# Optimization experiments

Hardware: AMD Instinct MI355X
Metric: run time of the kernel (lower is better)

Reference implementation:

```python
import jax, jax.numpy as jnp
import numpy as np

N_NODES = 50000

def cheb_conv(x, edge_index, W, b):
    # PyG ChebConv, K=2, normalization='sym', lambda_max=2.0 (default):
    # scaled Laplacian L_hat = (2/lambda_max)*L - I = -D^{-1/2} A D^{-1/2} (zero diag).
    # Tx_0 = x, Tx_1 = L_hat @ x ; out = Tx_0 @ W[0] + Tx_1 @ W[1] + b
    src, dst = edge_index[0], edge_index[1]
    ones = jnp.ones(src.shape[0], x.dtype)
    deg = jax.ops.segment_sum(ones, src, num_segments=N_NODES)
    dinv = jnp.where(deg > 0, 1.0 / jnp.sqrt(deg), 0.0)
    norm = -dinv[src] * dinv[dst]                                   # [E]
    tx1 = jax.ops.segment_sum(x[src] * norm[:, None], dst, num_segments=N_NODES)
    return x @ W[0] + tx1 @ W[1] + b

def setup_inputs() -> dict:
    key = jax.random.key(0)
    ks = jax.random.split(key, 12)
    IN, OUT, E, P = 128, 2, 800000, 400000
    return {
        "x": jax.random.normal(ks[0], (N_NODES, IN), jnp.float32),
        "edge_index": jax.random.randint(ks[1], (2, E), 0, N_NODES),
        "E_pos": jax.random.randint(ks[2], (2, P), 0, N_NODES),
        "neg_edge_index": jax.random.randint(ks[3], (2, P), 0, N_NODES),
        "W1": jax.random.normal(ks[4], (2, IN, 300), jnp.float32) * 0.05,
        "b1": jnp.zeros((300,), jnp.float32),
        "W2": jax.random.normal(ks[5], (2, 300, 100), jnp.float32) * 0.05,
        "b2": jnp.zeros((100,), jnp.float32),
        "W3": jax.random.normal(ks[6], (2, 100, OUT), jnp.float32) * 0.05,
        "b3": jnp.zeros((OUT,), jnp.float32),
        "lin1_W": jax.random.normal(ks[7], (100, IN), jnp.float32) * 0.05,
        "lin1_b": jnp.zeros((100,), jnp.float32),
        "lin2_W": jax.random.normal(ks[8], (100, IN), jnp.float32) * 0.05,
        "lin2_b": jnp.zeros((100,), jnp.float32),
        "c1": jnp.full((1,), 0.5, jnp.float32),
        "c2": jnp.full((1,), 0.5, jnp.float32),
    }

def reference(x, edge_index, E_pos, neg_edge_index, W1, b1, W2, b2, W3, b3,
              lin1_W, lin1_b, lin2_W, lin2_b, c1, c2):
    # eval mode: F.dropout and dropout_edge are identity
    x0 = x
    h = jax.nn.relu(cheb_conv(x0, edge_index, W1, b1))
    x1 = jax.nn.relu(cheb_conv(h, edge_index, W2, b2))
    x2 = x1 + jax.nn.relu(x0 @ lin1_W.T + lin1_b)
    z = x1 + jax.nn.relu(x0 @ lin2_W.T + lin2_b)
    pos_score = jnp.sum(z[E_pos[0]] * z[E_pos[1]], axis=1)              # [P]
    pos_loss = -jnp.mean(jnp.log(jax.nn.sigmoid(pos_score) + 1e-15))
    neg_score = jnp.sum(z[neg_edge_index[0]] * z[neg_edge_index[1]], axis=1)
    neg_loss = -jnp.mean(jnp.log(1.0 - jax.nn.sigmoid(neg_score) + 1e-15))
    r_loss = pos_loss + neg_loss
    out = cheb_conv(x2, edge_index, W3, b3)                             # [N, out_channels]
    return (out, r_loss, c1, c2)
```

## Files before the change

### kernel.cpp

```cpp
#include <hip/hip_runtime.h>
#include <math.h>


typedef unsigned short ushort_t;
typedef unsigned char u8;
typedef __attribute__((ext_vector_type(8))) __bf16 bf16x8;
typedef __attribute__((ext_vector_type(8))) short s16x8;
typedef __attribute__((ext_vector_type(4))) float f32x4;
typedef __attribute__((ext_vector_type(2))) float f32x2;

#define NB_H 64
#define HW 12500

__device__ __forceinline__ f32x4 mfma16x16x32(s16x8 a, s16x8 b, f32x4 c) {
  return __builtin_amdgcn_mfma_f32_16x16x32_bf16(
      __builtin_bit_cast(bf16x8, a), __builtin_bit_cast(bf16x8, b), c, 0, 0, 0);
}
__device__ __forceinline__ ushort_t f2bf(float f) {
  union { float f; unsigned u; } c; c.f = f;
  unsigned r = (c.u + 0x7FFFu + ((c.u >> 16) & 1u)) >> 16;
  return (ushort_t)r;
}
__device__ __forceinline__ f32x2 cvt2lo(unsigned u) {
  return __builtin_amdgcn_cvt_pk_f32_fp8((int)u, false);
}
__device__ __forceinline__ f32x2 cvt2hi(unsigned u) {
  return __builtin_amdgcn_cvt_pk_f32_fp8((int)u, true);
}
__device__ __forceinline__ u8 f2fp8(float f) {
  return (u8)(__builtin_amdgcn_cvt_pk_fp8_f32(f, 0.f, 0, false) & 0xff);
}

template<int VAR, int NT, int KTOT>
__global__ __launch_bounds__(256) void gemm_mfma(
    const ushort_t* __restrict__ A0, const ushort_t* __restrict__ A1,
    const ushort_t* __restrict__ Wt,
    const float* __restrict__ bias0, const float* __restrict__ bias1,
    const float* __restrict__ x1,
    const float* __restrict__ W3c, const float* __restrict__ b3c,
    void* __restrict__ out0, void* __restrict__ out1,
    float* __restrict__ t0g, float* __restrict__ t1g, int M,
    int gemmNB,
    const int* __restrict__ ep, const int* __restrict__ en, int P,
    const int* __restrict__ pptr, const unsigned* __restrict__ baseP,
    const ushort_t* __restrict__ prank, int2* __restrict__ psr)
{
  if (VAR == 0 && (int)blockIdx.x >= gemmNB) {
    const int i = ((int)blockIdx.x - gemmNB) * 256 + (int)threadIdx.x;
    const int twoP = 2 * P;
    if (i >= twoP) return;
    const int neg = (i >= P);
    const int p = neg ? i - P : i;
    const int* ia = neg ? en : ep;
    const int na = ia[p], nbv = ia[P + p];
    const int cs2 = (twoP + NB_H - 1) / NB_H;
    const int b = i / cs2;
    const unsigned bv = baseP[(size_t)b * HW + (na >> 2)];
    const int base = (int)((bv >> ((na & 3) * 8)) & 0xffu);
    const int pos = pptr[na] + base + (int)prank[i];
    psr[pos] = make_int2(na, nbv | (neg ? (int)0x80000000 : 0));
    return;
  }
  constexpr int NF = NT / 32;
  __shared__ __align__(16) ushort_t As[64 * 40];
  __shared__ __align__(16) ushort_t Bs[NT * 40];
  __shared__ float w3s[400];
  const int tid  = threadIdx.x;
  const int lane = tid & 63, w = tid >> 6;
  const int m0 = blockIdx.x * 64;
  const int wm = (w & 1) * 32, wn = (w >> 1) * (NT / 2);
  if (VAR == 2) { for (int i = tid; i < 400; i += 256) w3s[i] = W3c[i]; }
  f32x4 acc[2][NF];
#pragma unroll
  for (int i = 0; i < 2; ++i)
#pragma unroll
    for (int j = 0; j < NF; ++j) acc[i][j] = (f32x4){0.f, 0.f, 0.f, 0.f};

  for (int k0 = 0; k0 < KTOT; k0 += 32) {
    {
      const int r = tid >> 2, c8 = (tid & 3) * 8;
      const int gm = m0 + r;
      uint4 v = {0u, 0u, 0u, 0u};
      if (gm < M) {
        if (VAR == 1) {
          const u8* s8 = (const u8*)A0 + (size_t)gm * 320 + k0 + c8;
          const uint2 r8 = *(const uint2*)s8;
          const f32x2 f0 = cvt2lo(r8.x), f1 = cvt2hi(r8.x);
          const f32x2 f2 = cvt2lo(r8.y), f3 = cvt2hi(r8.y);
          v.x = (unsigned)f2bf(f0.x) | ((unsigned)f2bf(f0.y) << 16);
          v.y = (unsigned)f2bf(f1.x) | ((unsigned)f2bf(f1.y) << 16);
          v.z = (unsigned)f2bf(f2.x) | ((unsigned)f2bf(f2.y) << 16);
          v.w = (unsigned)f2bf(f3.x) | ((unsigned)f2bf(f3.y) << 16);
        } else {
          const ushort_t* srcp;
          if (VAR == 0) srcp = (k0 < 128) ? A0 + (size_t)gm * 128 + k0 + c8
                                          : A1 + (size_t)gm * 128 + (k0 - 128) + c8;
          else srcp = A0 + (size_t)gm * 128 + k0 + c8;
          v = *(const uint4*)srcp;
        }
      }
      *(uint4*)&As[r * 40 + c8] = v;
    }
    {
      const int c8 = (tid & 3) * 8;
#pragma unroll
      for (int i = 0; i < (NT * 4 + 255) / 256; ++i) {
        const int r = (tid >> 2) + i * 64;
        if (r < NT)
          *(uint4*)&Bs[r * 40 + c8] = *(const uint4*)(Wt + (size_t)r * KTOT + k0 + c8);
      }
    }
    __syncthreads();
    s16x8 af[2], bfr[NF];
#pragma unroll
    for (int mi = 0; mi < 2; ++mi)
      af[mi] = *(const s16x8*)&As[(wm + mi * 16 + (lane & 15)) * 40 + (lane >> 4) * 8];
#pragma unroll
    for (int ni = 0; ni < NF; ++ni)
      bfr[ni] = *(const s16x8*)&Bs[(wn + ni * 16 + (lane & 15)) * 40 + (lane >> 4) * 8];
#pragma unroll
    for (int mi = 0; mi < 2; ++mi)
#pragma unroll
      for (int ni = 0; ni < NF; ++ni)
        acc[mi][ni] = mfma16x16x32(af[mi], bfr[ni], acc[mi][ni]);
    __syncthreads();
  }

  if (VAR == 2) {
#pragma unroll
    for (int mi = 0; mi < 2; ++mi)
#pragma unroll
      for (int r = 0; r < 4; ++r) {
        const int gRow = m0 + wm + mi * 16 + ((lane >> 4) << 2) + r;
        float p0 = 0.f, p1 = 0.f, p2 = 0.f, p3 = 0.f;
#pragma unroll
        for (int ni = 0; ni < NF; ++ni) {
          const int col = wn + ni * 16 + (lane & 15);
          const float v = acc[mi][ni][r];
          if (gRow < M) {
            if (col < 100) {
              const float x2v = x1[(size_t)gRow * 128 + col] + fmaxf(v + bias0[col], 0.f);
              p0 = fmaf(x2v, w3s[col * 2 + 0], p0);
              p1 = fmaf(x2v, w3s[col * 2 + 1], p1);
              p2 = fmaf(x2v, w3s[200 + col * 2 + 0], p2);
              p3 = fmaf(x2v, w3s[200 + col * 2 + 1], p3);
            } else if (col < 200) {
              const int c = col - 100;
              ((u8*)out1)[(size_t)gRow * 128 + c] =
                  f2fp8(x1[(size_t)gRow * 128 + c] + fmaxf(v + bias1[c], 0.f));
            }
          }
        }
        if (wn == 0) {
#pragma unroll
          for (int off = 8; off; off >>= 1) {
            p0 += __shfl_down(p0, off, 16);
            p1 += __shfl_down(p1, off, 16);
            p2 += __shfl_down(p2, off, 16);
            p3 += __shfl_down(p3, off, 16);
          }
          if ((lane & 15) == 0 && gRow < M) {
            t0g[(size_t)gRow * 2 + 0] = p0 + b3c[0];
            t0g[(size_t)gRow * 2 + 1] = p1 + b3c[1];
            t1g[(size_t)gRow * 2 + 0] = p2;
            t1g[(size_t)gRow * 2 + 1] = p3;
          }
        }
      }
  } else {
#pragma unroll
    for (int mi = 0; mi < 2; ++mi)
#pragma unroll
      for (int ni = 0; ni < NF; ++ni)
#pragma unroll
        for (int r = 0; r < 4; ++r) {
          const int gRow = m0 + wm + mi * 16 + ((lane >> 4) << 2) + r;
          const int col  = wn + ni * 16 + (lane & 15);
          if (gRow >= M) continue;
          const float v = acc[mi][ni][r];
          if (VAR == 0) {
            ((u8*)out0)[(size_t)gRow * 320 + col] =
                (col < 300) ? f2fp8(fmaxf(v + bias0[col], 0.f)) : (u8)0;
          } else {
            if (col < 100) ((float*)out0)[(size_t)gRow * 128 + col] = v + bias0[col];
            else if (col < 200) ((u8*)out1)[(size_t)gRow * 128 + (col - 100)] = f2fp8(v);
          }
        }
  }
}

__global__ __launch_bounds__(256) void prep(
    const int* __restrict__ src, const int* __restrict__ dst, int E, int M,
    unsigned* __restrict__ partS, unsigned* __restrict__ partD,
    ushort_t* __restrict__ rank,
    const int* __restrict__ ep, const int* __restrict__ en, int P,
    unsigned* __restrict__ partP, ushort_t* __restrict__ prank,
    const float* __restrict__ x, ushort_t* __restrict__ xb,
    u8* __restrict__ xf8, int n4,
    const float* __restrict__ W1, const float* __restrict__ W2,
    const float* __restrict__ l1W, const float* __restrict__ l2W,
    ushort_t* __restrict__ W1t, ushort_t* __restrict__ W2t,
    ushort_t* __restrict__ Wlt)
{
  __shared__ unsigned hist[HW];
  const int blk = blockIdx.x;
  if (blk < 2 * NB_H) {
    const int isD = (blk >= NB_H);
    const int b = isD ? blk - NB_H : blk;
    const int* keys = isD ? dst : src;
    unsigned* part = isD ? partD : partS;
    const int cs = (E + NB_H - 1) / NB_H;
    const int e0 = b * cs;
    const int e1 = (e0 + cs < E) ? e0 + cs : E;
    for (int i = threadIdx.x; i < HW; i += 256) hist[i] = 0;
    __syncthreads();
    for (int e = e0 + threadIdx.x; e < e1; e += 256) {
      const int k = keys[e];
      const unsigned old = atomicAdd(&hist[k >> 2], 1u << ((k & 3) * 8));
      if (isD) rank[e] = (ushort_t)((old >> ((k & 3) * 8)) & 0xffu);
    }
    __syncthreads();
    for (int i = threadIdx.x; i < HW; i += 256)
      part[(size_t)b * HW + i] = hist[i];
    return;
  }
  if (blk < 3 * NB_H) {
    const int b = blk - 2 * NB_H;
    const int twoP = 2 * P;
    const int cs2 = (twoP + NB_H - 1) / NB_H;
    const int e0 = b * cs2;
    const int e1 = (e0 + cs2 < twoP) ? e0 + cs2 : twoP;
    for (int i = threadIdx.x; i < HW; i += 256) hist[i] = 0;
    __syncthreads();
    for (int i = e0 + threadIdx.x; i < e1; i += 256) {
      const int neg = (i >= P);
      const int p = neg ? i - P : i;
      const int* ia = neg ? en : ep;
      const int k = ia[p];
      const unsigned old = atomicAdd(&hist[k >> 2], 1u << ((k & 3) * 8));
      prank[i] = (ushort_t)((old >> ((k & 3) * 8)) & 0xffu);
    }
    __syncthreads();
    for (int i = threadIdx.x; i < HW; i += 256)
      partP[(size_t)b * HW + i] = hist[i];
    return;
  }
  const int i = (blk - 3 * NB_H) * 256 + threadIdx.x;
  if (i < n4) {
    const float4 v = ((const float4*)x)[i];
    ushort4 o; o.x = f2bf(v.x); o.y = f2bf(v.y); o.z = f2bf(v.z); o.w = f2bf(v.w);
    ((ushort4*)xb)[i] = o;
    int p = 0;
    p = __builtin_amdgcn_cvt_pk_fp8_f32(v.x, v.y, p, false);
    p = __builtin_amdgcn_cvt_pk_fp8_f32(v.z, v.w, p, true);
    ((unsigned*)xf8)[i] = (unsigned)p;
    return;
  }
  const int j = i - n4;
  if (j < 81920) {
    const int n = j >> 8, k = j & 255;
    float v = 0.f;
    if (n < 300) v = (k < 128) ? W1[k * 300 + n] : W1[38400 + (k - 128) * 300 + n];
    W1t[j] = f2bf(v);
  } else if (j < 153600) {
    const int jj = j - 81920;
    const int n = jj / 320, k = jj - n * 320;
    float v = 0.f;
    if (n < 200 && k < 300) v = W2[(n < 100 ? 0 : 30000) + k * 100 + (n % 100)];
    W2t[jj] = f2bf(v);
  } else if (j < 182272) {
    const int jj = j - 153600;
    const int n = jj >> 7, k = jj & 127;
    float v = 0.f;
    if (n < 100) v = l1W[n * 128 + k];
    else if (n < 200) v = l2W[(n - 100) * 128 + k];
    Wlt[jj] = f2bf(v);
  }
}

__global__ void scan_local(const unsigned* __restrict__ partS,
                           unsigned* __restrict__ partD,
                           unsigned* __restrict__ partP,
                           float* __restrict__ dinv,
                           int* __restrict__ ptr, int* __restrict__ pptr,
                           int* __restrict__ bsumE, int* __restrict__ bsumP, int n)
{
  __shared__ int tmp[256];
  const int i = blockIdx.x * 256 + threadIdx.x;
  const int lane = threadIdx.x & 63;
  unsigned ssum = 0, dtot = 0, ptot = 0;
  if (i < n && (i & 3) == 0) {
    const int c = i >> 2;
    for (int b = 0; b < NB_H; b += 8) {
      unsigned sv[8];
#pragma unroll
      for (int q = 0; q < 8; ++q) sv[q] = partS[(size_t)(b + q) * HW + c];
#pragma unroll
      for (int q = 0; q < 8; ++q) ssum += sv[q];
    }
    unsigned run = 0;
    for (int b = 0; b < NB_H; b += 8) {
      unsigned dv[8];
#pragma unroll
      for (int q = 0; q < 8; ++q) dv[q] = partD[(size_t)(b + q) * HW + c];
#pragma unroll
      for (int q = 0; q < 8; ++q) { const unsigned pre = run; run += dv[q]; dv[q] = pre; }
#pragma unroll
      for (int q = 0; q < 8; ++q) partD[(size_t)(b + q) * HW + c] = dv[q];
    }
    dtot = run;
    unsigned prun = 0;
    for (int b = 0; b < NB_H; b += 8) {
      unsigned pv[8];
#pragma unroll
      for (int q = 0; q < 8; ++q) pv[q] = partP[(size_t)(b + q) * HW + c];
#pragma unroll
      for (int q = 0; q < 8; ++q) { const unsigned pre = prun; prun += pv[q]; pv[q] = pre; }
#pragma unroll
      for (int q = 0; q < 8; ++q) partP[(size_t)(b + q) * HW + c] = pv[q];
    }
    ptot = prun;
  }
  const unsigned sAll = __shfl(ssum, lane & ~3, 64);
  const unsigned dAll = __shfl(dtot, lane & ~3, 64);
  const unsigned pAll = __shfl(ptot, lane & ~3, 64);
  int v = 0, v2 = 0;
  if (i < n) {
    const int hs = (i & 3) * 8;
    const unsigned dg = (sAll >> hs) & 0xffu;
    dinv[i] = dg ? 1.f / sqrtf((float)dg) : 0.f;
    v = (int)((dAll >> hs) & 0xffu);
    v2 = (int)((pAll >> hs) & 0xffu);
  }
  tmp[threadIdx.x] = v;
  __syncthreads();
  for (int off = 1; off < 256; off <<= 1) {
    const int t = (threadIdx.x >= off) ? tmp[threadIdx.x - off] : 0;
    __syncthreads();
    tmp[threadIdx.x] += t;
    __syncthreads();
  }
  if (i < n) ptr[i] = tmp[threadIdx.x] - v;
  if (threadIdx.x == 255) bsumE[blockIdx.x] = tmp[255];
  __syncthreads();
  tmp[threadIdx.x] = v2;
  __syncthreads();
  for (int off = 1; off < 256; off <<= 1) {
    const int t = (threadIdx.x >= off) ? tmp[threadIdx.x - off] : 0;
    __syncthreads();
    tmp[threadIdx.x] += t;
    __syncthreads();
  }
  if (i < n) pptr[i] = tmp[threadIdx.x] - v2;
  if (threadIdx.x == 255) bsumP[blockIdx.x] = tmp[255];
}

__global__ void scan_add2(int* __restrict__ ptr, int* __restrict__ pptr,
                          const int* __restrict__ bsumE, const int* __restrict__ bsumP,
                          int n, int E, int twoP, int nb, float* __restrict__ accs)
{
  __shared__ int tmp[256];
  const int v = (threadIdx.x < nb) ? bsumE[threadIdx.x] : 0;
  tmp[threadIdx.x] = v;
  __syncthreads();
  for (int off = 1; off < 256; off <<= 1) {
    const int t = (threadIdx.x >= off) ? tmp[threadIdx.x - off] : 0;
    __syncthreads();
    tmp[threadIdx.x] += t;
    __syncthreads();
  }
  const int offE = (blockIdx.x > 0) ? tmp[blockIdx.x - 1] : 0;
  __syncthreads();
  const int v2 = (threadIdx.x < nb) ? bsumP[threadIdx.x] : 0;
  tmp[threadIdx.x] = v2;
  __syncthreads();
  for (int off = 1; off < 256; off <<= 1) {
    const int t = (threadIdx.x >= off) ? tmp[threadIdx.x - off] : 0;
    __syncthreads();
    tmp[threadIdx.x] += t;
    __syncthreads();
  }
  const int offP = (blockIdx.x > 0) ? tmp[blockIdx.x - 1] : 0;
  const int i = blockIdx.x * 256 + threadIdx.x;
  if (i < n) { ptr[i] += offE; pptr[i] += offP; }
  if (i == 0) { ptr[n] = E; pptr[n] = twoP; accs[0] = 0.f; accs[1] = 0.f; }
}

__global__ void fill_csr2(const int* __restrict__ src, const int* __restrict__ dst,
                          const float* __restrict__ dinv, const int* __restrict__ ptr,
                          const unsigned* __restrict__ baseD,
                          const ushort_t* __restrict__ rank,
                          int2* __restrict__ csr, int E)
{
  const int e = blockIdx.x * 256 + threadIdx.x;
  if (e >= E) return;
  const int cs = (E + NB_H - 1) / NB_H;
  const int b = e / cs;
  const int s = src[e], d = dst[e];
  const unsigned bv = baseD[(size_t)b * HW + (d >> 2)];
  const int base = (int)((bv >> ((d & 3) * 8)) & 0xffu);
  const int pos = ptr[d] + base + (int)rank[e];
  const float w = -dinv[s] * dinv[d];
  csr[pos] = make_int2(s, __float_as_int(w));
}

#define ACCV(u, ww) { f32x2 t; \
  t = cvt2lo(u.x); a[0]  = fmaf(ww, t.x, a[0]);  a[1]  = fmaf(ww, t.y, a[1]);  \
  t = cvt2hi(u.x); a[2]  = fmaf(ww, t.x, a[2]);  a[3]  = fmaf(ww, t.y, a[3]);  \
  t = cvt2lo(u.y); a[4]  = fmaf(ww, t.x, a[4]);  a[5]  = fmaf(ww, t.y, a[5]);  \
  t = cvt2hi(u.y); a[6]  = fmaf(ww, t.x, a[6]);  a[7]  = fmaf(ww, t.y, a[7]);  \
  t = cvt2lo(u.z); a[8]  = fmaf(ww, t.x, a[8]);  a[9]  = fmaf(ww, t.y, a[9]);  \
  t = cvt2hi(u.z); a[10] = fmaf(ww, t.x, a[10]); a[11] = fmaf(ww, t.y, a[11]); \
  t = cvt2lo(u.w); a[12] = fmaf(ww, t.x, a[12]); a[13] = fmaf(ww, t.y, a[13]); \
  t = cvt2hi(u.w); a[14] = fmaf(ww, t.x, a[14]); a[15] = fmaf(ww, t.y, a[15]); }

__global__ __launch_bounds__(256) void gather128e(
    const u8* __restrict__ xf8, ushort_t* __restrict__ txb,
    const int* __restrict__ ptr, const int2* __restrict__ csr, int M)
{
  const int node = (blockIdx.x * 256 + threadIdx.x) >> 3;
  const int sub  = threadIdx.x & 7;
  if (node >= M) return;
  const int beg = ptr[node], end = ptr[node + 1];
  float a[16] = {};
  int p = beg;
  for (; p + 8 <= end; p += 8) {
    int2 e[8];
#pragma unroll
    for (int q = 0; q < 8; ++q) e[q] = csr[p + q];
    uint4 v[8];
#pragma unroll
    for (int q = 0; q < 8; ++q)
      v[q] = *(const uint4*)(xf8 + (size_t)e[q].x * 128 + sub * 16);
#pragma unroll
    for (int q = 0; q < 8; ++q) { const float wq = __int_as_float(e[q].y); ACCV(v[q], wq) }
  }
  for (; p < end; ++p) {
    const int2 eq = csr[p]; const float wq = __int_as_float(eq.y);
    const uint4 v = *(const uint4*)(xf8 + (size_t)eq.x * 128 + sub * 16);
    ACCV(v, wq)
  }
  uint4 o1, o2;
  o1.x = (unsigned)f2bf(a[0])  | ((unsigned)f2bf(a[1])  << 16);
  o1.y = (unsigned)f2bf(a[2])  | ((unsigned)f2bf(a[3])  << 16);
  o1.z = (unsigned)f2bf(a[4])  | ((unsigned)f2bf(a[5])  << 16);
  o1.w = (unsigned)f2bf(a[6])  | ((unsigned)f2bf(a[7])  << 16);
  o2.x = (unsigned)f2bf(a[8])  | ((unsigned)f2bf(a[9])  << 16);
  o2.y = (unsigned)f2bf(a[10]) | ((unsigned)f2bf(a[11]) << 16);
  o2.z = (unsigned)f2bf(a[12]) | ((unsigned)f2bf(a[13]) << 16);
  o2.w = (unsigned)f2bf(a[14]) | ((unsigned)f2bf(a[15]) << 16);
  ushort_t* dstp = txb + (size_t)node * 128 + sub * 16;
  *(uint4*)dstp = o1;
  *(uint4*)(dstp + 8) = o2;
}

__global__ __launch_bounds__(256) void gather100e_x1(
    const u8* __restrict__ Brh, float* __restrict__ Ar,
    const int* __restrict__ ptr, const int2* __restrict__ csr, int M)
{
  const int node = (blockIdx.x * 256 + threadIdx.x) >> 3;
  const int sub  = threadIdx.x & 7;
  if (node >= M) return;
  const int beg = ptr[node], end = ptr[node + 1];
  float a[16] = {};
  int p = beg;
  for (; p + 8 <= end; p += 8) {
    int2 e[8];
#pragma unroll
    for (int q = 0; q < 8; ++q) e[q] = csr[p + q];
    uint4 v[8];
#pragma unroll
    for (int q = 0; q < 8; ++q)
      v[q] = *(const uint4*)(Brh + (size_t)e[q].x * 128 + sub * 16);
#pragma unroll
    for (int q = 0; q < 8; ++q) { const float wq = __int_as_float(e[q].y); ACCV(v[q], wq) }
  }
  for (; p < end; ++p) {
    const int2 eq = csr[p]; const float wq = __int_as_float(eq.y);
    const uint4 v = *(const uint4*)(Brh + (size_t)eq.x * 128 + sub * 16);
    ACCV(v, wq)
  }
  float* dstp = Ar + (size_t)node * 128 + sub * 16;
#pragma unroll
  for (int q = 0; q < 4; ++q) {
    float4 b = *(const float4*)(dstp + q * 4);
    b.x = fmaxf(b.x + a[q * 4 + 0], 0.f);
    b.y = fmaxf(b.y + a[q * 4 + 1], 0.f);
    b.z = fmaxf(b.z + a[q * 4 + 2], 0.f);
    b.w = fmaxf(b.w + a[q * 4 + 3], 0.f);
    *(float4*)(dstp + q * 4) = b;
  }
}
#undef ACCV

__device__ __forceinline__ void maskrow(uint4& r, int sub) {
  if (sub >= 6) { r.y = 0u; r.z = 0u; r.w = 0u; if (sub == 7) r.x = 0u; }
}
#define DOTA(vv, s) { f32x2 q_; \
  q_ = cvt2lo(vv.x); s = fmaf(af[0],  q_.x, s); s = fmaf(af[1],  q_.y, s); \
  q_ = cvt2hi(vv.x); s = fmaf(af[2],  q_.x, s); s = fmaf(af[3],  q_.y, s); \
  q_ = cvt2lo(vv.y); s = fmaf(af[4],  q_.x, s); s = fmaf(af[5],  q_.y, s); \
  q_ = cvt2hi(vv.y); s = fmaf(af[6],  q_.x, s); s = fmaf(af[7],  q_.y, s); \
  q_ = cvt2lo(vv.z); s = fmaf(af[8],  q_.x, s); s = fmaf(af[9],  q_.y, s); \
  q_ = cvt2hi(vv.z); s = fmaf(af[10], q_.x, s); s = fmaf(af[11], q_.y, s); \
  q_ = cvt2lo(vv.w); s = fmaf(af[12], q_.x, s); s = fmaf(af[13], q_.y, s); \
  q_ = cvt2hi(vv.w); s = fmaf(af[14], q_.x, s); s = fmaf(af[15], q_.y, s); }
#define CVT_AF(ra) { f32x2 t_; \
  t_ = cvt2lo(ra.x); af[0]  = t_.x; af[1]  = t_.y; \
  t_ = cvt2hi(ra.x); af[2]  = t_.x; af[3]  = t_.y; \
  t_ = cvt2lo(ra.y); af[4]  = t_.x; af[5]  = t_.y; \
  t_ = cvt2hi(ra.y); af[6]  = t_.x; af[7]  = t_.y; \
  t_ = cvt2lo(ra.z); af[8]  = t_.x; af[9]  = t_.y; \
  t_ = cvt2hi(ra.z); af[10] = t_.x; af[11] = t_.y; \
  t_ = cvt2lo(ra.w); af[12] = t_.x; af[13] = t_.y; \
  t_ = cvt2hi(ra.w); af[14] = t_.x; af[15] = t_.y; }

__global__ __launch_bounds__(256) void loss_g2(
    const u8* __restrict__ zf8, const int2* __restrict__ psr,
    float* __restrict__ acc,
    const float* __restrict__ t1, const float* __restrict__ t0,
    const int* __restrict__ ptr, const int2* __restrict__ csr,
    float* __restrict__ out, int M, int twoP, int nbScan)
{
  const int tid = threadIdx.x;
  if ((int)blockIdx.x < nbScan) {
    const int i = blockIdx.x * 256 + tid;
    if (i >= M) return;
    float a0 = 0.f, a1 = 0.f;
    const int beg = ptr[i], end = ptr[i + 1];
    int p = beg;
    for (; p + 4 <= end; p += 4) {
      const int2 e0 = csr[p], e1 = csr[p + 1], e2 = csr[p + 2], e3 = csr[p + 3];
      const float w0 = __int_as_float(e0.y), w1 = __int_as_float(e1.y);
      const float w2 = __int_as_float(e2.y), w3 = __int_as_float(e3.y);
      const float2 v0 = *(const float2*)(t1 + (size_t)e0.x * 2);
      const float2 v1 = *(const float2*)(t1 + (size_t)e1.x * 2);
      const float2 v2 = *(const float2*)(t1 + (size_t)e2.x * 2);
      const float2 v3 = *(const float2*)(t1 + (size_t)e3.x * 2);
      a0 = fmaf(w0, v0.x, a0); a1 = fmaf(w0, v0.y, a1);
      a0 = fmaf(w1, v1.x, a0); a1 = fmaf(w1, v1.y, a1);
      a0 = fmaf(w2, v2.x, a0); a1 = fmaf(w2, v2.y, a1);
      a0 = fmaf(w3, v3.x, a0); a1 = fmaf(w3, v3.y, a1);
    }
    for (; p < end; ++p) {
      const int2 eq = csr[p]; const float wq = __int_as_float(eq.y);
      const float2 v = *(const float2*)(t1 + (size_t)eq.x * 2);
      a0 = fmaf(wq, v.x, a0); a1 = fmaf(wq, v.y, a1);
    }
    const float2 base = *(const float2*)(t0 + (size_t)i * 2);
    *(float2*)(out + (size_t)i * 2) = make_float2(base.x + a0, base.y + a1);
    return;
  }
  __shared__ float red[8];
  const int lane = tid & 63, wib = tid >> 6;
  const int sub = tid & 7;
  const int slot = ((int)blockIdx.x - nbScan) * 32 + (tid >> 3);
  float tp = 0.f, tn = 0.f;
  int p = slot * 16;
  if (p < twoP) {
    const int pend = (p + 16 < twoP) ? p + 16 : twoP;
    int curNa = -1;
    float af[16];
#pragma unroll
    for (int q = 0; q < 16; ++q) af[q] = 0.f;
    for (; p + 4 <= pend; p += 4) {
      int2 pr4[4];
#pragma unroll
      for (int q = 0; q < 4; ++q) pr4[q] = psr[p + q];
      uint4 rb[4];
#pragma unroll
      for (int q = 0; q < 4; ++q) {
        rb[q] = make_uint4(0u, 0u, 0u, 0u);
        const int nv = pr4[q].y & 0x7fffffff;
        if (sub < 7) rb[q] = *(const uint4*)(zf8 + (size_t)nv * 128 + sub * 16);
        maskrow(rb[q], sub);
      }
      float s[4] = {0.f, 0.f, 0.f, 0.f};
#pragma unroll
      for (int q = 0; q < 4; ++q) {
        if (pr4[q].x != curNa) {
          curNa = pr4[q].x;
          uint4 ra = make_uint4(0u, 0u, 0u, 0u);
          if (sub < 7) ra = *(const uint4*)(zf8 + (size_t)curNa * 128 + sub * 16);
          maskrow(ra, sub);
          CVT_AF(ra)
        }
        DOTA(rb[q], s[q])
      }
#pragma unroll
      for (int off = 4; off; off >>= 1) {
#pragma unroll
        for (int q = 0; q < 4; ++q) s[q] += __shfl_down(s[q], off, 8);
      }
      if (sub == 0) {
#pragma unroll
        for (int q = 0; q < 4; ++q) {
          const float sig = 1.f / (1.f + __expf(-s[q]));
          if ((unsigned)pr4[q].y >> 31) tn += __logf(1.f - sig + 1e-15f);
          else tp += __logf(sig + 1e-15f);
        }
      }
    }
    for (; p < pend; ++p) {
      const int2 pr = psr[p];
      const int nv = pr.y & 0x7fffffff;
      uint4 rb = make_uint4(0u, 0u, 0u, 0u);
      if (sub < 7) rb = *(const uint4*)(zf8 + (size_t)nv * 128 + sub * 16);
      maskrow(rb, sub);
      if (pr.x != curNa) {
        curNa = pr.x;
        uint4 ra = make_uint4(0u, 0u, 0u, 0u);
        if (sub < 7) ra = *(const uint4*)(zf8 + (size_t)curNa * 128 + sub * 16);
        maskrow(ra, sub);
        CVT_AF(ra)
      }
      float s = 0.f;
      DOTA(rb, s)
#pragma unroll
      for (int off = 4; off; off >>= 1) s += __shfl_down(s, off, 8);
      if (sub == 0) {
        const float sig = 1.f / (1.f + __expf(-s));
        if ((unsigned)pr.y >> 31) tn += __logf(1.f - sig + 1e-15f);
        else tp += __logf(sig + 1e-15f);
      }
    }
  }
  tp += __shfl_down(tp, 32, 64); tn += __shfl_down(tn, 32, 64);
  tp += __shfl_down(tp, 16, 64); tn += __shfl_down(tn, 16, 64);
  tp += __shfl_down(tp, 8, 64);  tn += __shfl_down(tn, 8, 64);
  if (lane == 0) { red[wib] = tp; red[4 + wib] = tn; }
  __syncthreads();
  if (tid == 0) {
    atomicAdd(acc + 0, red[0] + red[1] + red[2] + red[3]);
    atomicAdd(acc + 1, red[4] + red[5] + red[6] + red[7]);
  }
}
#undef DOTA
#undef CVT_AF

__global__ void final_scalars(const float* __restrict__ accs,
                              const float* __restrict__ c1, const float* __restrict__ c2,
                              float* __restrict__ out, int M, float invP)
{
  out[2 * M + 0] = -(accs[0] + accs[1]) * invP;
  out[2 * M + 1] = c1[0];
  out[2 * M + 2] = c2[0];
}

extern "C" void kernel_launch(void* const* d_in, const int* in_sizes, int n_in,
                              void* d_out, int out_size, void* d_ws, size_t ws_size,
                              hipStream_t stream)
{
  const float* x   = (const float*)d_in[0];
  const int*   ei  = (const int*)d_in[1];
  const int*   ep  = (const int*)d_in[2];
  const int*   en  = (const int*)d_in[3];
  const float* W1  = (const float*)d_in[4];
  const float* b1  = (const float*)d_in[5];
  const float* W2  = (const float*)d_in[6];
  const float* b2  = (const float*)d_in[7];
  const float* W3  = (const float*)d_in[8];
  const float* b3  = (const float*)d_in[9];
  const float* l1W = (const float*)d_in[10];
  const float* l1b = (const float*)d_in[11];
  const float* l2W = (const float*)d_in[12];
  const float* l2b = (const float*)d_in[13];
  const float* c1  = (const float*)d_in[14];
  const float* c2  = (const float*)d_in[15];
  float* out = (float*)d_out;

  const int M = in_sizes[0] / 128;
  const int E = in_sizes[1] / 2;
  const int P = in_sizes[2] / 2;
  const int* src = ei;
  const int* dst = ei + E;
  const int nb_scan = (M + 255) / 256;
  const int fillE = (E + 255) / 256;
  const int fillP = (2 * P + 255) / 256;
  const int lossSlots = (2 * P + 15) / 16;
  const int lossNB = (lossSlots + 31) / 32;

  float* ws = (float*)d_ws;
  size_t o = 0;
  float*    dinv = ws + o;            o += 50176;
  int*      ptr  = (int*)(ws + o);    o += (size_t)M + 8;
  int*      pptr = (int*)(ws + o);    o += (size_t)M + 8;
  int*      bsumE = (int*)(ws + o);   o += 256;
  int*      bsumP = (int*)(ws + o);   o += 256;
  int2*     csr  = (int2*)(ws + o);   o += (size_t)E * 2;
  ushort_t* rank = (ushort_t*)(ws + o); o += (size_t)E / 2;
  int2*     psr  = (int2*)(ws + o);   o += (size_t)4 * P;
  ushort_t* xb   = (ushort_t*)(ws + o); o += (size_t)M * 64;
  u8*       xf8  = (u8*)(ws + o);     o += (size_t)M * 32;
  ushort_t* tx0b = (ushort_t*)(ws + o); o += (size_t)M * 64;
  ushort_t* W1t  = (ushort_t*)(ws + o); o += 40960;
  ushort_t* W2t  = (ushort_t*)(ws + o); o += 35840;
  ushort_t* Wlt  = (ushort_t*)(ws + o); o += 14336;
  u8*       h8   = (u8*)(ws + o);     o += (size_t)M * 160;
  float*    Ar   = ws + o;            o += (size_t)M * 128;
  u8*       Brh  = (u8*)(ws + o);     o += (size_t)M * 32;
  u8*       zf8  = (u8*)(ws + o);     o += (size_t)M * 32;
  float*    t0   = ws + o;            o += (size_t)M * 2;
  float*    t1   = ws + o;            o += (size_t)M * 2;
  float*    accs = ws + o;            o += 8;
  unsigned* partS = (unsigned*)h8;
  unsigned* partD = (unsigned*)Ar;
  unsigned* partP = (unsigned*)Ar + 800000;
  ushort_t* prank = (ushort_t*)((unsigned*)Ar + 1600000);

  const int n4 = M * 32;
  const int packBlocks = (n4 + 182272 + 255) / 256;
  prep<<<3 * NB_H + packBlocks, 256, 0, stream>>>(
      src, dst, E, M, partS, partD, rank,
      ep, en, P, partP, prank,
      x, xb, xf8, n4, W1, W2, l1W, l2W, W1t, W2t, Wlt);

  scan_local<<<nb_scan, 256, 0, stream>>>(partS, partD, partP, dinv, ptr, pptr,
                                          bsumE, bsumP, M);
  scan_add2<<<nb_scan, 256, 0, stream>>>(ptr, pptr, bsumE, bsumP, M, E, 2 * P,
                                         nb_scan, accs);
  fill_csr2<<<fillE, 256, 0, stream>>>(src, dst, dinv, ptr, partD, rank, csr, E);

  const int gB = (M + 63) / 64;
  const int gE8 = (M * 8 + 255) / 256;

  gather128e<<<gE8, 256, 0, stream>>>(xf8, tx0b, ptr, csr, M);
  gemm_mfma<0, 320, 256><<<gB + fillP, 256, 0, stream>>>(
      xb, tx0b, W1t, b1, nullptr, nullptr, nullptr, nullptr, h8, nullptr,
      nullptr, nullptr, M, gB, ep, en, P, pptr, partP, prank, psr);

  gemm_mfma<1, 224, 320><<<gB, 256, 0, stream>>>(
      (const ushort_t*)h8, nullptr, W2t, b2, nullptr, nullptr, nullptr, nullptr,
      Ar, Brh, nullptr, nullptr, M, gB, nullptr, nullptr, 0, nullptr, nullptr,
      nullptr, nullptr);
  gather100e_x1<<<gE8, 256, 0, stream>>>(Brh, Ar, ptr, csr, M);

  gemm_mfma<2, 224, 128><<<gB, 256, 0, stream>>>(
      xb, nullptr, Wlt, l1b, l2b, Ar , W3, b3, nullptr, zf8, t0, t1, M,
      gB, nullptr, nullptr, 0, nullptr, nullptr, nullptr, nullptr);

  loss_g2<<<nb_scan + lossNB, 256, 0, stream>>>(
      zf8, psr, accs, t1, t0, ptr, csr, out, M, 2 * P, nb_scan);
  final_scalars<<<1, 1, 0, stream>>>(accs, c1, c2, out, M, 1.0f / (float)P);
}
```

Baseline: 442.2 us.

## Split pair-scatter across two GEMM launches and fold final scalars into loss kernel

Splits the positive/negative pair CSR scatter blocks between the first and second GEMM launches, so each GEMM hides half of that work. Relocates partP/prank scratch into the h8 region past M*320 bytes so they no longer alias Ar, which the second GEMM now writes while the scatter still reads them. Removes the final_scalars launch by having the last loss block, found with an atomic ticket counter, write the loss and c1/c2. This saves a kernel launch but adds fences and a counter atomic per block, and relies on the new scratch layout fitting within h8.

```diff
diff --git a/kernel.cpp b/kernel.cpp
--- a/kernel.cpp
+++ b/kernel.cpp
@@ -40,13 +40,13 @@
     const float* __restrict__ W3c, const float* __restrict__ b3c,
     void* __restrict__ out0, void* __restrict__ out1,
     float* __restrict__ t0g, float* __restrict__ t1g, int M,
-    int gemmNB,
+    int gemmNB, int pfOff,
     const int* __restrict__ ep, const int* __restrict__ en, int P,
     const int* __restrict__ pptr, const unsigned* __restrict__ baseP,
     const ushort_t* __restrict__ prank, int2* __restrict__ psr)
 {
-  if (VAR == 0 && (int)blockIdx.x >= gemmNB) {
-    const int i = ((int)blockIdx.x - gemmNB) * 256 + (int)threadIdx.x;
+  if (VAR != 2 && (int)blockIdx.x >= gemmNB) {
+    const int i = ((int)blockIdx.x - gemmNB) * 256 + (int)threadIdx.x + pfOff;
     const int twoP = 2 * P;
     if (i >= twoP) return;
     const int neg = (i >= P);
@@ -383,7 +383,10 @@
   const int offP = (blockIdx.x > 0) ? tmp[blockIdx.x - 1] : 0;
   const int i = blockIdx.x * 256 + threadIdx.x;
   if (i < n) { ptr[i] += offE; pptr[i] += offP; }
-  if (i == 0) { ptr[n] = E; pptr[n] = twoP; accs[0] = 0.f; accs[1] = 0.f; }
+  if (i == 0) {
+    ptr[n] = E; pptr[n] = twoP;
+    accs[0] = 0.f; accs[1] = 0.f; accs[4] = 0.f;
+  }
 }
 
 __global__ void fill_csr2(const int* __restrict__ src, const int* __restrict__ dst,
@@ -520,7 +523,8 @@
     float* __restrict__ acc,
     const float* __restrict__ t1, const float* __restrict__ t0,
     const int* __restrict__ ptr, const int2* __restrict__ csr,
-    float* __restrict__ out, int M, int twoP, int nbScan)
+    float* __restrict__ out, int M, int twoP, int nbScan, int lossNB,
+    const float* __restrict__ c1, const float* __restrict__ c2, float invP)
 {
   const int tid = threadIdx.x;
   if ((int)blockIdx.x < nbScan) {
@@ -633,19 +637,20 @@
   if (tid == 0) {
     atomicAdd(acc + 0, red[0] + red[1] + red[2] + red[3]);
     atomicAdd(acc + 1, red[4] + red[5] + red[6] + red[7]);
+    __threadfence();
+    const unsigned t = atomicAdd((unsigned*)(acc + 4), 1u);
+    if (t == (unsigned)(lossNB - 1)) {
+      __threadfence();
+      const float a0 = atomicAdd(acc + 0, 0.f);
+      const float a1 = atomicAdd(acc + 1, 0.f);
+      out[2 * M + 0] = -(a0 + a1) * invP;
+      out[2 * M + 1] = c1[0];
+      out[2 * M + 2] = c2[0];
+    }
   }
 }
 #undef DOTA
 #undef CVT_AF
-
-__global__ void final_scalars(const float* __restrict__ accs,
-                              const float* __restrict__ c1, const float* __restrict__ c2,
-                              float* __restrict__ out, int M, float invP)
-{
-  out[2 * M + 0] = -(accs[0] + accs[1]) * invP;
-  out[2 * M + 1] = c1[0];
-  out[2 * M + 2] = c2[0];
-}
 
 extern "C" void kernel_launch(void* const* d_in, const int* in_sizes, int n_in,
                               void* d_out, int out_size, void* d_ws, size_t ws_size,
@@ -677,6 +682,8 @@
   const int nb_scan = (M + 255) / 256;
   const int fillE = (E + 255) / 256;
   const int fillP = (2 * P + 255) / 256;
+  const int pf0 = fillP / 2;
+  const int pf1 = fillP - pf0;
   const int lossSlots = (2 * P + 15) / 16;
   const int lossNB = (lossSlots + 31) / 32;
 
@@ -705,8 +712,8 @@
   float*    accs = ws + o;            o += 8;
   unsigned* partS = (unsigned*)h8;
   unsigned* partD = (unsigned*)Ar;
-  unsigned* partP = (unsigned*)Ar + 800000;
-  ushort_t* prank = (ushort_t*)((unsigned*)Ar + 1600000);
+  unsigned* partP = (unsigned*)(h8 + (size_t)M * 320);
+  ushort_t* prank = (ushort_t*)(h8 + (size_t)M * 320 + 3200000);
 
   const int n4 = M * 32;
   const int packBlocks = (n4 + 182272 + 255) / 256;
@@ -725,21 +732,21 @@
   const int gE8 = (M * 8 + 255) / 256;
 
   gather128e<<<gE8, 256, 0, stream>>>(xf8, tx0b, ptr, csr, M);
-  gemm_mfma<0, 320, 256><<<gB + fillP, 256, 0, stream>>>(
+  gemm_mfma<0, 320, 256><<<gB + pf0, 256, 0, stream>>>(
       xb, tx0b, W1t, b1, nullptr, nullptr, nullptr, nullptr, h8, nullptr,
-      nullptr, nullptr, M, gB, ep, en, P, pptr, partP, prank, psr);
-
-  gemm_mfma<1, 224, 320><<<gB, 256, 0, stream>>>(
+      nullptr, nullptr, M, gB, 0, ep, en, P, pptr, partP, prank, psr);
+
+  gemm_mfma<1, 224, 320><<<gB + pf1, 256, 0, stream>>>(
       (const ushort_t*)h8, nullptr, W2t, b2, nullptr, nullptr, nullptr, nullptr,
-      Ar, Brh, nullptr, nullptr, M, gB, nullptr, nullptr, 0, nullptr, nullptr,
-      nullptr, nullptr);
+      Ar, Brh, nullptr, nullptr, M, gB, pf0 * 256, ep, en, P, pptr, partP,
+      prank, psr);
   gather100e_x1<<<gE8, 256, 0, stream>>>(Brh, Ar, ptr, csr, M);
 
   gemm_mfma<2, 224, 128><<<gB, 256, 0, stream>>>(
       xb, nullptr, Wlt, l1b, l2b, Ar , W3, b3, nullptr, zf8, t0, t1, M,
-      gB, nullptr, nullptr, 0, nullptr, nullptr, nullptr, nullptr);
+      gB, 0, nullptr, nullptr, 0, nullptr, nullptr, nullptr, nullptr);
 
   loss_g2<<<nb_scan + lossNB, 256, 0, stream>>>(
-      zf8, psr, accs, t1, t0, ptr, csr, out, M, 2 * P, nb_scan);
-  final_scalars<<<1, 1, 0, stream>>>(accs, c1, c2, out, M, 1.0f / (float)P);
-}
+      zf8, psr, accs, t1, t0, ptr, csr, out, M, 2 * P, nb_scan, lossNB,
+      c1, c2, 1.0f / (float)P);
+}
```

Result: slower. 467.9 us (+5.8%).
